# Optimization experiments

Hardware: AMD Instinct MI355X
Metric: run time of the kernel (lower is better)

Reference implementation:

```python
import jax, jax.numpy as jnp
import numpy as np

H = 1024
LENGTH = 48
N = 2048


def setup_inputs() -> dict:
    key = jax.random.key(0)
    k1, k2, k3, k4 = jax.random.split(key, 4)
    s = 1.0 / np.sqrt(H)  # torch LSTMCell init: U(-1/sqrt(H), 1/sqrt(H))
    h_in = jax.random.normal(k1, (N, H), dtype=jnp.float32)
    W_hh = jax.random.uniform(k2, (4 * H, H), minval=-s, maxval=s, dtype=jnp.float32)
    b_ih = jax.random.uniform(k3, (4 * H,), minval=-s, maxval=s, dtype=jnp.float32)
    b_hh = jax.random.uniform(k4, (4 * H,), minval=-s, maxval=s, dtype=jnp.float32)
    return {"h_in": h_in, "W_hh": W_hh, "b_ih": b_ih, "b_hh": b_hh}


def reference(h_in, W_hh, b_ih, b_hh):
    # LSTMCell with input_size=0: gates depend only on hidden state.
    # torch gate order: i, f, g, o.
    Hd = h_in.shape[1]
    bias = b_ih + b_hh
    c0 = jnp.zeros_like(h_in)

    def step(carry, _):
        h, c = carry
        z = h @ W_hh.T + bias  # (N, 4H)
        i = jax.nn.sigmoid(z[:, :Hd])
        f = jax.nn.sigmoid(z[:, Hd:2 * Hd])
        g = jnp.tanh(z[:, 2 * Hd:3 * Hd])
        o = jax.nn.sigmoid(z[:, 3 * Hd:])
        c_new = f * c + i * g
        h_new = o * jnp.tanh(c_new)
        return (h_new, c_new), h_new

    _, hs = jax.lax.scan(step, (h_in, c0), None, length=LENGTH)  # (L, N, H)
    return jnp.transpose(hs, (1, 2, 0))  # (N, H, L) matching torch.stack(axis=-1)
```

## Files before the change

kernel.cpp:

```cpp
#include <hip/hip_runtime.h>
#include <hip/hip_bf16.h>

#define Hdim 1024
#define Nb   2048
#define Lsteps 48

typedef unsigned short ushort_t;
typedef short bf16x8 __attribute__((ext_vector_type(8)));
typedef float f32x4 __attribute__((ext_vector_type(4)));

typedef __attribute__((address_space(3))) unsigned int lds_u32;
typedef const __attribute__((address_space(1))) unsigned int glb_u32;

__device__ __forceinline__ void gll16(const void* g, void* l) {
    __builtin_amdgcn_global_load_lds((glb_u32*)g, (lds_u32*)l, 16, 0, 0);
}

__device__ __forceinline__ ushort_t f2bf(float x) {
    unsigned u = __builtin_bit_cast(unsigned, x);
    unsigned r = u + 0x7fffu + ((u >> 16) & 1u);
    return (ushort_t)(r >> 16);
}

__device__ __forceinline__ float fsigmoid(float x) {
    return 1.0f / (1.0f + __expf(-x));
}
__device__ __forceinline__ float ftanh(float x) {
    float xm = fminf(fmaxf(x, -15.0f), 15.0f);
    float e = __expf(2.0f * xm);
    return (e - 1.0f) / (e + 1.0f);
}

__device__ __forceinline__ f32x4 mfma16(bf16x8 a, bf16x8 b, f32x4 c) {
    return __builtin_amdgcn_mfma_f32_16x16x32_bf16(a, b, c, 0, 0, 0);
}

__global__ __launch_bounds__(256) void prep_w(const float* __restrict__ W,
                                              ushort_t* __restrict__ Wb) {
    int i = blockIdx.x * 256 + threadIdx.x;
    Wb[i] = f2bf(W[i]);
}

__global__ __launch_bounds__(256) void prep_h(const float* __restrict__ h_in,
                                              ushort_t* __restrict__ h0,
                                              const float* __restrict__ b_ih,
                                              const float* __restrict__ b_hh,
                                              float* __restrict__ bias) {
    int i = blockIdx.x * 256 + threadIdx.x;
    h0[i] = f2bf(h_in[i]);
    if (i < 4 * Hdim) bias[i] = b_ih[i] + b_hh[i];
}

__global__ __launch_bounds__(256) void lstm_step(
    const ushort_t* __restrict__ hsrc,
    ushort_t* __restrict__ hdst,
    const ushort_t* __restrict__ Wb,
    const float* __restrict__ bias,
    float* __restrict__ cst,
    float* __restrict__ tmp)
{
    __shared__ __align__(16) ushort_t As[128 * 64];
    __shared__ __align__(16) ushort_t Bs[128 * 64];

    const int tid  = threadIdx.x;
    const int lane = tid & 63;
    const int wid  = tid >> 6;
    const int wr   = wid >> 1;
    const int wc   = wid & 1;

    const int p    = blockIdx.x;
    const int xcd  = p & 7;
    const int slot = p >> 3;
    const int jb   = (xcd >> 1) * 8 + (slot & 7);
    const int nb   = (xcd & 1) * 8 + (slot >> 3);
    const int n0   = nb * 128;
    const int j0   = jb * 32;

    f32x4 acc[4][4];
#pragma unroll
    for (int g = 0; g < 4; ++g)
#pragma unroll
        for (int ri = 0; ri < 4; ++ri)
            acc[g][ri] = (f32x4){0.f, 0.f, 0.f, 0.f};

    const int srow8  = lane >> 3;
    const int schunk = (lane & 7) ^ srow8;
    const int choff  = schunk * 8;

    const ushort_t* aGlob = hsrc + (size_t)(n0 + wid * 32 + srow8) * Hdim + choff;
    const ushort_t* bGlob = Wb + (size_t)(wid * Hdim + j0 + srow8) * Hdim + choff;

    const int lr   = lane & 15;
    const int rsw  = lr & 7;
    const int cq   = lane >> 4;

    for (int it = 0; it < 16; ++it) {
        const int k0 = it * 64;
        __syncthreads();
#pragma unroll
        for (int ii = 0; ii < 4; ++ii) {
            gll16(aGlob + (size_t)ii * 8 * Hdim + k0, &As[(wid * 32 + ii * 8) * 64]);
        }
#pragma unroll
        for (int ii = 0; ii < 4; ++ii) {
            gll16(bGlob + (size_t)ii * 8 * Hdim + k0, &Bs[(wid * 32 + ii * 8) * 64]);
        }
        __syncthreads();

#pragma unroll
        for (int kh = 0; kh < 2; ++kh) {
            const int ch = ((cq + kh * 4) ^ rsw) * 8;
            bf16x8 af[4], bfr[4];
#pragma unroll
            for (int ri = 0; ri < 4; ++ri) {
                int row = wr * 64 + ri * 16 + lr;
                af[ri] = *(const bf16x8*)&As[row * 64 + ch];
            }
#pragma unroll
            for (int g = 0; g < 4; ++g) {
                int u = g * 32 + wc * 16 + lr;
                bfr[g] = *(const bf16x8*)&Bs[u * 64 + ch];
            }
#pragma unroll
            for (int g = 0; g < 4; ++g)
#pragma unroll
                for (int ri = 0; ri < 4; ++ri)
                    acc[g][ri] = mfma16(af[ri], bfr[g], acc[g][ri]);
        }
    }

    const int q4 = (lane >> 4) * 4;
    const int j  = j0 + wc * 16 + lr;
    const float bi = bias[j];
    const float bf = bias[Hdim + j];
    const float bg = bias[2 * Hdim + j];
    const float bo = bias[3 * Hdim + j];
#pragma unroll
    for (int ri = 0; ri < 4; ++ri)
#pragma unroll
        for (int q = 0; q < 4; ++q) {
            int n = n0 + wr * 64 + ri * 16 + q4 + q;
            float gi = fsigmoid(acc[0][ri][q] + bi);
            float gf = fsigmoid(acc[1][ri][q] + bf);
            float gg = ftanh(acc[2][ri][q] + bg);
            float go = fsigmoid(acc[3][ri][q] + bo);
            size_t idx = (size_t)n * Hdim + j;
            float cn = gf * cst[idx] + gi * gg;
            cst[idx] = cn;
            float hv = go * ftanh(cn);
            hdst[idx] = f2bf(hv);
            tmp[idx] = hv;
        }
}

__global__ __launch_bounds__(256) void flush16(const float* __restrict__ tmp,
                                               float* __restrict__ out, int t0) {
    int idx = blockIdx.x * 256 + threadIdx.x;
    float v[16];
#pragma unroll
    for (int s = 0; s < 16; ++s)
        v[s] = tmp[(size_t)s * (Nb * Hdim) + idx];
    float4* dst = (float4*)(out + (size_t)idx * Lsteps + t0);
#pragma unroll
    for (int s = 0; s < 4; ++s)
        dst[s] = make_float4(v[4 * s], v[4 * s + 1], v[4 * s + 2], v[4 * s + 3]);
}

extern "C" void kernel_launch(void* const* d_in, const int* in_sizes, int n_in,
                              void* d_out, int out_size, void* d_ws, size_t ws_size,
                              hipStream_t stream) {
    const float* h_in = (const float*)d_in[0];
    const float* W    = (const float*)d_in[1];
    const float* b_ih = (const float*)d_in[2];
    const float* b_hh = (const float*)d_in[3];
    float* out = (float*)d_out;

    char* ws = (char*)d_ws;
    ushort_t* Wb   = (ushort_t*)(ws);
    ushort_t* h0   = (ushort_t*)(ws + 8388608);
    ushort_t* h1   = (ushort_t*)(ws + 12582912);
    float*    cst  = (float*)(ws + 16777216);
    float*    bias = (float*)(ws + 25165824);
    float*    tmp16= (float*)(ws + 25182208);

    hipMemsetAsync(cst, 0, (size_t)Nb * Hdim * sizeof(float), stream);

    prep_w<<<(4 * Hdim * Hdim) / 256, 256, 0, stream>>>(W, Wb);
    prep_h<<<(Nb * Hdim) / 256, 256, 0, stream>>>(h_in, h0, b_ih, b_hh, bias);

    for (int t = 0; t < Lsteps; ++t) {
        const ushort_t* hs = (t & 1) ? h1 : h0;
        ushort_t*       hd = (t & 1) ? h0 : h1;
        float* tslot = tmp16 + (size_t)(t & 15) * (Nb * Hdim);
        lstm_step<<<512, 256, 0, stream>>>(hs, hd, Wb, bias, cst, tslot);
        if ((t & 15) == 15) {
            flush16<<<(Nb * Hdim) / 256, 256, 0, stream>>>(tmp16, out, t - 15);
        }
    }
}
```

Before: 1.885 ms.

## Double-buffer LDS tiles in LSTM step GEMM and use fast reciprocal

Splits the shared-memory A/B tiles into two buffers so the global-to-LDS loads for the next K chunk are issued before computing on the current chunk, halving the barriers per iteration and overlapping memory latency with MFMA work. Also replaces the divisions in sigmoid and tanh with a hardware reciprocal approximation. Doubling LDS to 64KB per block may lower occupancy, and the approximate reciprocal slightly changes numerical accuracy.

```diff
diff --git a/kernel.cpp b/kernel.cpp
--- a/kernel.cpp
+++ b/kernel.cpp
@@ -22,13 +22,15 @@
     return (ushort_t)(r >> 16);
 }
 
+__device__ __forceinline__ float frcp(float x) { return __builtin_amdgcn_rcpf(x); }
+
 __device__ __forceinline__ float fsigmoid(float x) {
-    return 1.0f / (1.0f + __expf(-x));
+    return frcp(1.0f + __expf(-x));
 }
 __device__ __forceinline__ float ftanh(float x) {
     float xm = fminf(fmaxf(x, -15.0f), 15.0f);
     float e = __expf(2.0f * xm);
-    return (e - 1.0f) / (e + 1.0f);
+    return (e - 1.0f) * frcp(e + 1.0f);
 }
 
 __device__ __forceinline__ f32x4 mfma16(bf16x8 a, bf16x8 b, f32x4 c) {
@@ -59,8 +61,8 @@
     float* __restrict__ cst,
     float* __restrict__ tmp)
 {
-    __shared__ __align__(16) ushort_t As[128 * 64];
-    __shared__ __align__(16) ushort_t Bs[128 * 64];
+    __shared__ __align__(16) ushort_t As[2][128 * 64];
+    __shared__ __align__(16) ushort_t Bs[2][128 * 64];
 
     const int tid  = threadIdx.x;
     const int lane = tid & 63;
@@ -94,19 +96,17 @@
     const int rsw  = lr & 7;
     const int cq   = lane >> 4;
 
-    for (int it = 0; it < 16; ++it) {
+    auto STAGE = [&](int buf, int it) {
         const int k0 = it * 64;
-        __syncthreads();
-#pragma unroll
-        for (int ii = 0; ii < 4; ++ii) {
-            gll16(aGlob + (size_t)ii * 8 * Hdim + k0, &As[(wid * 32 + ii * 8) * 64]);
-        }
-#pragma unroll
-        for (int ii = 0; ii < 4; ++ii) {
-            gll16(bGlob + (size_t)ii * 8 * Hdim + k0, &Bs[(wid * 32 + ii * 8) * 64]);
-        }
-        __syncthreads();
-
+#pragma unroll
+        for (int ii = 0; ii < 4; ++ii)
+            gll16(aGlob + (size_t)ii * 8 * Hdim + k0, &As[buf][(wid * 32 + ii * 8) * 64]);
+#pragma unroll
+        for (int ii = 0; ii < 4; ++ii)
+            gll16(bGlob + (size_t)ii * 8 * Hdim + k0, &Bs[buf][(wid * 32 + ii * 8) * 64]);
+    };
+
+    auto COMPUTE = [&](int buf) {
 #pragma unroll
         for (int kh = 0; kh < 2; ++kh) {
             const int ch = ((cq + kh * 4) ^ rsw) * 8;
@@ -114,12 +114,12 @@
 #pragma unroll
             for (int ri = 0; ri < 4; ++ri) {
                 int row = wr * 64 + ri * 16 + lr;
-                af[ri] = *(const bf16x8*)&As[row * 64 + ch];
+                af[ri] = *(const bf16x8*)&As[buf][row * 64 + ch];
             }
 #pragma unroll
             for (int g = 0; g < 4; ++g) {
                 int u = g * 32 + wc * 16 + lr;
-                bfr[g] = *(const bf16x8*)&Bs[u * 64 + ch];
+                bfr[g] = *(const bf16x8*)&Bs[buf][u * 64 + ch];
             }
 #pragma unroll
             for (int g = 0; g < 4; ++g)
@@ -127,7 +127,23 @@
                 for (int ri = 0; ri < 4; ++ri)
                     acc[g][ri] = mfma16(af[ri], bfr[g], acc[g][ri]);
         }
+    };
+
+    STAGE(0, 0);
+    __syncthreads();
+#pragma unroll 1
+    for (int it = 0; it < 14; it += 2) {
+        STAGE(1, it + 1);
+        COMPUTE(0);
+        __syncthreads();
+        STAGE(0, it + 2);
+        COMPUTE(1);
+        __syncthreads();
     }
+    STAGE(1, 15);
+    COMPUTE(0);
+    __syncthreads();
+    COMPUTE(1);
 
     const int q4 = (lane >> 4) * 4;
     const int j  = j0 + wc * 16 + lr;
```

Result: faster. 1.777 ms (-5.7%).
